# Optimization experiments

Measured on AMD Instinct MI355X. Metric: run time of the kernel, lower is better.

The kernel has to match this reference:

```python
import jax, jax.numpy as jnp
import numpy as np

MAX_SPAN_LEN = 20
LN_EPS = 1e-12


def _layer_norm(x, g, b):
    mu = jnp.mean(x, axis=-1, keepdims=True)
    var = jnp.mean(jnp.square(x - mu), axis=-1, keepdims=True)
    return (x - mu) * jax.lax.rsqrt(var + LN_EPS) * g + b


def _gelu(x):
    return jax.nn.gelu(x, approximate=False)  # exact BERT gelu


def setup_inputs() -> dict:
    key = jax.random.key(0)
    ks = jax.random.split(key, 8)
    bs, seq_len, dim = 8, 512, 768
    num_pairs, pe, emb, vocab = 32, 200, 128, 30522
    d_in = 2 * dim + pe
    s = lambda n: 1.0 / np.sqrt(n)
    return {
        "hidden_states": jax.random.normal(ks[0], (bs, seq_len, dim), jnp.float32),
        "pairs": jax.random.randint(ks[1], (bs, num_pairs, 2), 0, seq_len, jnp.int64 if jax.config.jax_enable_x64 else jnp.int32),
        "pos_emb": jax.random.normal(ks[2], (MAX_SPAN_LEN, pe), jnp.float32) * 0.02,
        "W1": jax.random.normal(ks[3], (d_in, dim), jnp.float32) * s(d_in),
        "b1": jnp.zeros((dim,), jnp.float32),
        "g1": jnp.ones((dim,), jnp.float32),
        "be1": jnp.zeros((dim,), jnp.float32),
        "W2": jax.random.normal(ks[4], (dim, dim), jnp.float32) * s(dim),
        "b2": jnp.zeros((dim,), jnp.float32),
        "g2": jnp.ones((dim,), jnp.float32),
        "be2": jnp.zeros((dim,), jnp.float32),
        "Wp": jax.random.normal(ks[5], (dim, emb), jnp.float32) * s(dim),
        "bp": jnp.zeros((emb,), jnp.float32),
        "Wdec": jax.random.normal(ks[6], (vocab, emb), jnp.float32) * 0.02,
    }


def reference(hidden_states, pairs, pos_emb, W1, b1, g1, be1, W2, b2, g2, be2, Wp, bp, Wdec):
    bs, num_pairs, _ = pairs.shape
    dim = hidden_states.shape[-1]
    # gather span endpoint hidden states: [bs, num_pairs, dim]
    left = jnp.take_along_axis(hidden_states, pairs[:, :, 0:1], axis=1) if False else None
    lh = jnp.take_along_axis(hidden_states, pairs[:, :, 0][..., None].astype(jnp.int32) * jnp.ones((1, 1, dim), jnp.int32), axis=1)
    rh = jnp.take_along_axis(hidden_states, pairs[:, :, 1][..., None].astype(jnp.int32) * jnp.ones((1, 1, dim), jnp.int32), axis=1)
    lh = lh.reshape(bs * num_pairs, 1, dim)
    rh = rh.reshape(bs * num_pairs, 1, dim)
    # broadcast over span positions and concat with position embeddings: [B*P, L, 2*dim+pe]
    B = bs * num_pairs
    L = MAX_SPAN_LEN
    x = jnp.concatenate([
        jnp.broadcast_to(lh, (B, L, dim)),
        jnp.broadcast_to(rh, (B, L, dim)),
        jnp.broadcast_to(pos_emb[None], (B, L, pos_emb.shape[-1])),
    ], axis=-1)
    h = _layer_norm(_gelu(x @ W1 + b1), g1, be1)
    h = _layer_norm(_gelu(h @ W2 + b2), g2, be2)
    h = h @ Wp + bp  # embeddings_project (embedding_size != hidden_size)
    return jnp.einsum("ble,ve->blv", h, Wdec)  # decoder, no bias
```

## Files before the change

kernel.cpp:

```cpp
#include <hip/hip_runtime.h>
#include <math.h>

#define DIM    768
#define PE     200
#define LSPAN  20
#define NPAIRS 256
#define ROWS   5120
#define EMB    128
#define VOCAB  30522

typedef __attribute__((ext_vector_type(8))) short short8;
typedef __attribute__((ext_vector_type(4))) float floatx4;

__device__ inline unsigned short f2bf(float f) {
    union { float f; unsigned int u; } v; v.f = f;
    unsigned int r = v.u + 0x7fffu + ((v.u >> 16) & 1u);
    return (unsigned short)(r >> 16);
}
__device__ inline float gelu_exact(float x) {
    return 0.5f * x * (1.0f + erff(x * 0.70710678118654752f));
}

__global__ void k_f32_to_bf16_vec4(const float* __restrict__ src, unsigned short* __restrict__ dst, int n4) {
    int i = blockIdx.x * blockDim.x + threadIdx.x;
    if (i >= n4) return;
    float4 v = ((const float4*)src)[i];
    ushort4 o;
    o.x = f2bf(v.x); o.y = f2bf(v.y); o.z = f2bf(v.z); o.w = f2bf(v.w);
    ((ushort4*)dst)[i] = o;
}

__global__ void k_transpose_bf16(const float* __restrict__ src, unsigned short* __restrict__ dst, int R, int C) {
    int i = blockIdx.x * blockDim.x + threadIdx.x;
    if (i >= R * C) return;
    int r = i / C, c = i % C;
    dst[c * R + r] = f2bf(src[i]);
}

__global__ __launch_bounds__(256) void k_posW(const float* __restrict__ pos_emb, const float* __restrict__ W1,
                                              const float* __restrict__ b1, float* __restrict__ posW) {
    __shared__ float pe_s[PE];
    int l = blockIdx.x, tid = threadIdx.x;
    if (tid < PE) pe_s[tid] = pos_emb[l * PE + tid];
    __syncthreads();
    for (int jj = 0; jj < 3; ++jj) {
        int j = jj * 256 + tid;
        float acc = b1[j];
        for (int k = 0; k < PE; ++k)
            acc += pe_s[k] * W1[(size_t)(2 * DIM + k) * DIM + j];
        posW[l * DIM + j] = acc;
    }
}

__global__ __launch_bounds__(256) void k_pairW(const float* __restrict__ hs, const int* __restrict__ pairs,
                                               const float* __restrict__ W1, float* __restrict__ pairW) {
    __shared__ float lh_s[4][DIM];
    __shared__ float rh_s[4][DIM];
    int tid = threadIdx.x;
    int jc = blockIdx.x;
    int g  = blockIdx.y;
    for (int p4 = 0; p4 < 4; ++p4) {
        int p = g * 4 + p4;
        int batch = p >> 5;
        int li = pairs[p * 2 + 0];
        int ri = pairs[p * 2 + 1];
        const float* lrow = hs + ((size_t)batch * 512 + li) * DIM;
        const float* rrow = hs + ((size_t)batch * 512 + ri) * DIM;
        for (int jj = 0; jj < 3; ++jj) {
            lh_s[p4][jj * 256 + tid] = lrow[jj * 256 + tid];
            rh_s[p4][jj * 256 + tid] = rrow[jj * 256 + tid];
        }
    }
    __syncthreads();
    int j = jc * 256 + tid;
    float a0 = 0.f, a1 = 0.f, a2 = 0.f, a3 = 0.f;
    for (int k = 0; k < DIM; ++k) {
        float w1a = W1[(size_t)k * DIM + j];
        float w1b = W1[(size_t)(DIM + k) * DIM + j];
        a0 += lh_s[0][k] * w1a + rh_s[0][k] * w1b;
        a1 += lh_s[1][k] * w1a + rh_s[1][k] * w1b;
        a2 += lh_s[2][k] * w1a + rh_s[2][k] * w1b;
        a3 += lh_s[3][k] * w1a + rh_s[3][k] * w1b;
    }
    pairW[(size_t)(g * 4 + 0) * DIM + j] = a0;
    pairW[(size_t)(g * 4 + 1) * DIM + j] = a1;
    pairW[(size_t)(g * 4 + 2) * DIM + j] = a2;
    pairW[(size_t)(g * 4 + 3) * DIM + j] = a3;
}

__global__ __launch_bounds__(256) void k_h1(const float* __restrict__ pairW, const float* __restrict__ posW,
                                            const float* __restrict__ g1, const float* __restrict__ be1,
                                            unsigned short* __restrict__ h1) {
    __shared__ float xs[DIM];
    __shared__ float red[10];
    int row = blockIdx.x, tid = threadIdx.x;
    int p = row / LSPAN, l = row % LSPAN;
    float s = 0.f, s2 = 0.f;
    for (int jj = 0; jj < 3; ++jj) {
        int j = jj * 256 + tid;
        float v = pairW[(size_t)p * DIM + j] + posW[l * DIM + j];
        float gv = gelu_exact(v);
        xs[j] = gv;
        s += gv; s2 += gv * gv;
    }
    for (int off = 32; off > 0; off >>= 1) { s += __shfl_down(s, off); s2 += __shfl_down(s2, off); }
    int w = tid >> 6, lane = tid & 63;
    if (lane == 0) { red[w] = s; red[4 + w] = s2; }
    __syncthreads();
    if (tid == 0) {
        float a = red[0] + red[1] + red[2] + red[3];
        float b = red[4] + red[5] + red[6] + red[7];
        float mu = a / DIM;
        float var = fmaxf(b / DIM - mu * mu, 0.f);
        red[8] = mu; red[9] = rsqrtf(var + 1e-12f);
    }
    __syncthreads();
    float mu = red[8], rstd = red[9];
    for (int jj = 0; jj < 3; ++jj) {
        int j = jj * 256 + tid;
        h1[(size_t)row * DIM + j] = f2bf((xs[j] - mu) * rstd * g1[j] + be1[j]);
    }
}

__global__ __launch_bounds__(256) void k_ln(const float* __restrict__ in, const float* __restrict__ gamma,
                                            const float* __restrict__ beta, unsigned short* __restrict__ out) {
    __shared__ float xs[DIM];
    __shared__ float red[10];
    int row = blockIdx.x, tid = threadIdx.x;
    float s = 0.f, s2 = 0.f;
    for (int jj = 0; jj < 3; ++jj) {
        int j = jj * 256 + tid;
        float v = in[(size_t)row * DIM + j];
        xs[j] = v;
        s += v; s2 += v * v;
    }
    for (int off = 32; off > 0; off >>= 1) { s += __shfl_down(s, off); s2 += __shfl_down(s2, off); }
    int w = tid >> 6, lane = tid & 63;
    if (lane == 0) { red[w] = s; red[4 + w] = s2; }
    __syncthreads();
    if (tid == 0) {
        float a = red[0] + red[1] + red[2] + red[3];
        float b = red[4] + red[5] + red[6] + red[7];
        float mu = a / DIM;
        float var = fmaxf(b / DIM - mu * mu, 0.f);
        red[8] = mu; red[9] = rsqrtf(var + 1e-12f);
    }
    __syncthreads();
    float mu = red[8], rstd = red[9];
    for (int jj = 0; jj < 3; ++jj) {
        int j = jj * 256 + tid;
        out[(size_t)row * DIM + j] = f2bf((xs[j] - mu) * rstd * gamma[j] + beta[j]);
    }
}

template <int EPI>
__global__ __launch_bounds__(256) void gemm_bt(const unsigned short* __restrict__ A,
                                               const unsigned short* __restrict__ B,
                                               const float* __restrict__ bias, void* __restrict__ Cout,
                                               int M, int N, int K, int ldc) {
    const int LDT = 136;
    __shared__ unsigned short As[64 * LDT];
    __shared__ unsigned short Bs[64 * LDT];
    int tid = threadIdx.x;
    int m0 = blockIdx.x * 64;
    int n0 = blockIdx.y * 64;
    int w = tid >> 6, lane = tid & 63;
    int quad = lane >> 4, r16 = lane & 15;
    int wm = (w >> 1) * 32, wn = (w & 1) * 32;

    floatx4 acc[2][2] = {};

    for (int k0 = 0; k0 < K; k0 += 128) {
#pragma unroll
        for (int i = 0; i < 4; ++i) {
            int c = tid + i * 256;
            int row = c >> 4;
            int kc = (c & 15) * 8;
            uint4 v = *(const uint4*)(&A[(size_t)(m0 + row) * K + k0 + kc]);
            *(uint4*)(&As[row * LDT + kc]) = v;
        }
#pragma unroll
        for (int i = 0; i < 4; ++i) {
            int c = tid + i * 256;
            int row = c >> 4;
            int kc = (c & 15) * 8;
            uint4 v = make_uint4(0u, 0u, 0u, 0u);
            if (n0 + row < N)
                v = *(const uint4*)(&B[(size_t)(n0 + row) * K + k0 + kc]);
            *(uint4*)(&Bs[row * LDT + kc]) = v;
        }
        __syncthreads();
#pragma unroll
        for (int kk = 0; kk < 4; ++kk) {
            short8 a0 = *(const short8*)(&As[(wm + 0 * 16 + r16) * LDT + kk * 32 + quad * 8]);
            short8 a1 = *(const short8*)(&As[(wm + 1 * 16 + r16) * LDT + kk * 32 + quad * 8]);
            short8 b0 = *(const short8*)(&Bs[(wn + 0 * 16 + r16) * LDT + kk * 32 + quad * 8]);
            short8 b1 = *(const short8*)(&Bs[(wn + 1 * 16 + r16) * LDT + kk * 32 + quad * 8]);
            acc[0][0] = __builtin_amdgcn_mfma_f32_16x16x32_bf16(a0, b0, acc[0][0], 0, 0, 0);
            acc[0][1] = __builtin_amdgcn_mfma_f32_16x16x32_bf16(a0, b1, acc[0][1], 0, 0, 0);
            acc[1][0] = __builtin_amdgcn_mfma_f32_16x16x32_bf16(a1, b0, acc[1][0], 0, 0, 0);
            acc[1][1] = __builtin_amdgcn_mfma_f32_16x16x32_bf16(a1, b1, acc[1][1], 0, 0, 0);
        }
        __syncthreads();
    }

#pragma unroll
    for (int mt = 0; mt < 2; ++mt)
#pragma unroll
        for (int nt = 0; nt < 2; ++nt)
#pragma unroll
            for (int r = 0; r < 4; ++r) {
                int row = m0 + wm + mt * 16 + quad * 4 + r;
                int col = n0 + wn + nt * 16 + r16;
                if (col < N) {
                    float v = acc[mt][nt][r];
                    if (EPI == 1) {
                        v = gelu_exact(v + bias[col]);
                        ((float*)Cout)[(size_t)row * ldc + col] = v;
                    } else if (EPI == 2) {
                        v += bias[col];
                        ((unsigned short*)Cout)[(size_t)row * ldc + col] = f2bf(v);
                    } else {
                        ((float*)Cout)[(size_t)row * ldc + col] = v;
                    }
                }
            }
}

extern "C" void kernel_launch(void* const* d_in, const int* in_sizes, int n_in,
                              void* d_out, int out_size, void* d_ws, size_t ws_size,
                              hipStream_t stream) {
    const float* hs      = (const float*)d_in[0];
    const int*   pairs   = (const int*)d_in[1];
    const float* pos_emb = (const float*)d_in[2];
    const float* W1      = (const float*)d_in[3];
    const float* b1      = (const float*)d_in[4];
    const float* g1      = (const float*)d_in[5];
    const float* be1     = (const float*)d_in[6];
    const float* W2      = (const float*)d_in[7];
    const float* b2      = (const float*)d_in[8];
    const float* g2      = (const float*)d_in[9];
    const float* be2     = (const float*)d_in[10];
    const float* Wp      = (const float*)d_in[11];
    const float* bp      = (const float*)d_in[12];
    const float* Wdec    = (const float*)d_in[13];
    float* out = (float*)d_out;

    char* ws = (char*)d_ws;
    float*          posW  = (float*)(ws + 0);
    float*          pairW = (float*)(ws + 61440);
    unsigned short* h1    = (unsigned short*)(ws + 847872);
    unsigned short* W2T   = (unsigned short*)(ws + 8712192);
    float*          y     = (float*)(ws + 9891840);
    unsigned short* h2    = (unsigned short*)(ws + 25620480);
    unsigned short* WpT   = (unsigned short*)(ws + 33484800);
    unsigned short* h3    = (unsigned short*)(ws + 33681408);
    unsigned short* WdecB = (unsigned short*)(ws + 34992128);

    int n4 = (VOCAB * EMB) / 4;
    k_f32_to_bf16_vec4<<<(n4 + 255) / 256, 256, 0, stream>>>(Wdec, WdecB, n4);
    k_transpose_bf16<<<(DIM * DIM + 255) / 256, 256, 0, stream>>>(W2, W2T, DIM, DIM);
    k_transpose_bf16<<<(DIM * EMB + 255) / 256, 256, 0, stream>>>(Wp, WpT, DIM, EMB);

    k_posW<<<LSPAN, 256, 0, stream>>>(pos_emb, W1, b1, posW);
    k_pairW<<<dim3(3, 64), 256, 0, stream>>>(hs, pairs, W1, pairW);
    k_h1<<<ROWS, 256, 0, stream>>>(pairW, posW, g1, be1, h1);

    gemm_bt<1><<<dim3(ROWS / 64, DIM / 64), 256, 0, stream>>>(h1, W2T, b2, y, ROWS, DIM, DIM, DIM);
    k_ln<<<ROWS, 256, 0, stream>>>(y, g2, be2, h2);

    gemm_bt<2><<<dim3(ROWS / 64, EMB / 64), 256, 0, stream>>>(h2, WpT, bp, h3, ROWS, EMB, DIM, EMB);

    gemm_bt<0><<<dim3(ROWS / 64, (VOCAB + 63) / 64), 256, 0, stream>>>(h3, WdecB, nullptr, out, ROWS, VOCAB, EMB, VOCAB);
}
```

Before: 980.9 us.

## Add dedicated decoder GEMM with XCD-aware tiling, tiled transpose, block swizzle

Replaces the generic decoder GEMM with a specialized kernel that uses 64x128 tiles and a single-shot K=128 load. Blocks are remapped so that each XCD processes a contiguous range of vocab panels, which should improve L2 reuse of the weight panels. The naive strided transposes of W2 and Wp become an LDS-tiled transpose, and gemm_bt gains a block-index swizzle across XCDs. The decoder GEMM writes a roughly 625MB fp32 output, so it is probably store-bound and the gains may be limited.

```diff
diff --git a/kernel.cpp b/kernel.cpp
--- a/kernel.cpp
+++ b/kernel.cpp
@@ -30,11 +30,25 @@
     ((ushort4*)dst)[i] = o;
 }
 
-__global__ void k_transpose_bf16(const float* __restrict__ src, unsigned short* __restrict__ dst, int R, int C) {
-    int i = blockIdx.x * blockDim.x + threadIdx.x;
-    if (i >= R * C) return;
-    int r = i / C, c = i % C;
-    dst[c * R + r] = f2bf(src[i]);
+__global__ __launch_bounds__(256) void k_transpose_bf16t(const float* __restrict__ src,
+                                                         unsigned short* __restrict__ dst,
+                                                         int R, int C) {
+    __shared__ float ls[64][65];
+    int r0 = blockIdx.x * 64, c0 = blockIdx.y * 64;
+    int tid = threadIdx.x;
+#pragma unroll
+    for (int i = 0; i < 16; ++i) {
+        int idx = tid + i * 256;
+        int lr = idx >> 6, lc = idx & 63;
+        ls[lr][lc] = src[(size_t)(r0 + lr) * C + c0 + lc];
+    }
+    __syncthreads();
+#pragma unroll
+    for (int i = 0; i < 16; ++i) {
+        int idx = tid + i * 256;
+        int oc = idx >> 6, orr = idx & 63;
+        dst[(size_t)(c0 + oc) * R + r0 + orr] = f2bf(ls[orr][oc]);
+    }
 }
 
 __global__ __launch_bounds__(256) void k_posW(const float* __restrict__ pos_emb, const float* __restrict__ W1,
@@ -162,7 +176,8 @@
     __shared__ unsigned short As[64 * LDT];
     __shared__ unsigned short Bs[64 * LDT];
     int tid = threadIdx.x;
-    int m0 = blockIdx.x * 64;
+    int bx = ((blockIdx.x & 7) * (gridDim.x >> 3)) + (blockIdx.x >> 3);
+    int m0 = bx * 64;
     int n0 = blockIdx.y * 64;
     int w = tid >> 6, lane = tid & 63;
     int quad = lane >> 4, r16 = lane & 15;
@@ -224,6 +239,78 @@
                         ((float*)Cout)[(size_t)row * ldc + col] = v;
                     }
                 }
+            }
+}
+
+#define DEC_NB  239
+#define DEC_MB  80
+#define DEC_NPX 30
+
+__global__ __launch_bounds__(256) void gemm_dec(const unsigned short* __restrict__ A,
+                                                const unsigned short* __restrict__ B,
+                                                float* __restrict__ C) {
+    const int LDT = 136;
+    __shared__ unsigned short As[64 * LDT];
+    __shared__ unsigned short Bs[128 * LDT];
+    int flat = blockIdx.x;
+    int xcd = flat & 7;
+    int j = flat >> 3;
+    int m = j % DEC_MB;
+    int npl = j / DEC_MB;
+    int npanel = xcd * DEC_NPX + npl;
+    if (npanel >= DEC_NB) return;
+    int m0 = m * 64;
+    int n0 = npanel * 128;
+    int tid = threadIdx.x;
+    int w = tid >> 6, lane = tid & 63;
+    int quad = lane >> 4, r16 = lane & 15;
+    int wm = (w >> 1) * 32, wn = (w & 1) * 64;
+
+#pragma unroll
+    for (int i = 0; i < 4; ++i) {
+        int c = tid + i * 256;
+        int row = c >> 4, kc = (c & 15) * 8;
+        *(uint4*)(&As[row * LDT + kc]) = *(const uint4*)(&A[(size_t)(m0 + row) * 128 + kc]);
+    }
+#pragma unroll
+    for (int i = 0; i < 8; ++i) {
+        int c = tid + i * 256;
+        int row = c >> 4, kc = (c & 15) * 8;
+        int brow = n0 + row;
+        if (brow >= VOCAB) brow = VOCAB - 1;
+        *(uint4*)(&Bs[row * LDT + kc]) = *(const uint4*)(&B[(size_t)brow * 128 + kc]);
+    }
+    __syncthreads();
+
+    floatx4 acc[2][4] = {};
+#pragma unroll
+    for (int kk = 0; kk < 4; ++kk) {
+        short8 a0 = *(const short8*)(&As[(wm + 0 * 16 + r16) * LDT + kk * 32 + quad * 8]);
+        short8 a1 = *(const short8*)(&As[(wm + 1 * 16 + r16) * LDT + kk * 32 + quad * 8]);
+        short8 b0 = *(const short8*)(&Bs[(wn + 0 * 16 + r16) * LDT + kk * 32 + quad * 8]);
+        short8 b1 = *(const short8*)(&Bs[(wn + 1 * 16 + r16) * LDT + kk * 32 + quad * 8]);
+        short8 b2 = *(const short8*)(&Bs[(wn + 2 * 16 + r16) * LDT + kk * 32 + quad * 8]);
+        short8 b3 = *(const short8*)(&Bs[(wn + 3 * 16 + r16) * LDT + kk * 32 + quad * 8]);
+        acc[0][0] = __builtin_amdgcn_mfma_f32_16x16x32_bf16(a0, b0, acc[0][0], 0, 0, 0);
+        acc[0][1] = __builtin_amdgcn_mfma_f32_16x16x32_bf16(a0, b1, acc[0][1], 0, 0, 0);
+        acc[0][2] = __builtin_amdgcn_mfma_f32_16x16x32_bf16(a0, b2, acc[0][2], 0, 0, 0);
+        acc[0][3] = __builtin_amdgcn_mfma_f32_16x16x32_bf16(a0, b3, acc[0][3], 0, 0, 0);
+        acc[1][0] = __builtin_amdgcn_mfma_f32_16x16x32_bf16(a1, b0, acc[1][0], 0, 0, 0);
+        acc[1][1] = __builtin_amdgcn_mfma_f32_16x16x32_bf16(a1, b1, acc[1][1], 0, 0, 0);
+        acc[1][2] = __builtin_amdgcn_mfma_f32_16x16x32_bf16(a1, b2, acc[1][2], 0, 0, 0);
+        acc[1][3] = __builtin_amdgcn_mfma_f32_16x16x32_bf16(a1, b3, acc[1][3], 0, 0, 0);
+    }
+
+#pragma unroll
+    for (int mt = 0; mt < 2; ++mt)
+#pragma unroll
+        for (int nt = 0; nt < 4; ++nt)
+#pragma unroll
+            for (int r = 0; r < 4; ++r) {
+                int row = m0 + wm + mt * 16 + quad * 4 + r;
+                int col = n0 + wn + nt * 16 + r16;
+                if (col < VOCAB)
+                    C[(size_t)row * VOCAB + col] = acc[mt][nt][r];
             }
 }
 
@@ -259,8 +346,8 @@
 
     int n4 = (VOCAB * EMB) / 4;
     k_f32_to_bf16_vec4<<<(n4 + 255) / 256, 256, 0, stream>>>(Wdec, WdecB, n4);
-    k_transpose_bf16<<<(DIM * DIM + 255) / 256, 256, 0, stream>>>(W2, W2T, DIM, DIM);
-    k_transpose_bf16<<<(DIM * EMB + 255) / 256, 256, 0, stream>>>(Wp, WpT, DIM, EMB);
+    k_transpose_bf16t<<<dim3(DIM / 64, DIM / 64), 256, 0, stream>>>(W2, W2T, DIM, DIM);
+    k_transpose_bf16t<<<dim3(DIM / 64, EMB / 64), 256, 0, stream>>>(Wp, WpT, DIM, EMB);
 
     k_posW<<<LSPAN, 256, 0, stream>>>(pos_emb, W1, b1, posW);
     k_pairW<<<dim3(3, 64), 256, 0, stream>>>(hs, pairs, W1, pairW);
@@ -271,5 +358,5 @@
 
     gemm_bt<2><<<dim3(ROWS / 64, EMB / 64), 256, 0, stream>>>(h2, WpT, bp, h3, ROWS, EMB, DIM, EMB);
 
-    gemm_bt<0><<<dim3(ROWS / 64, (VOCAB + 63) / 64), 256, 0, stream>>>(h3, WdecB, nullptr, out, ROWS, VOCAB, EMB, VOCAB);
-}
+    gemm_dec<<<8 * DEC_NPX * DEC_MB, 256, 0, stream>>>(h3, WdecB, out);
+}
```

Measured after the change: 970.5 us. Within noise of the previous version (-1.1%).
